# Kernel tuning notes

Hardware: AMD Instinct MI355X
Metric: run time of the kernel (lower is better)

Reference implementation:

```python
import jax, jax.numpy as jnp
import numpy as np

B, H, N, D = 4, 16, 4096, 64
M = 266  # nb_features = int(D * ln(D))
KERNEL_EPS = 1e-4


def _gaussian_orthogonal_random_matrix(nb_rows, nb_cols, rng):
    # Faithful to gaussian_orthogonal_random_matrix with scaling=0.
    blocks = []
    for _ in range(nb_rows // nb_cols):
        q, _ = np.linalg.qr(rng.standard_normal((nb_cols, nb_cols)))
        blocks.append(q.T)
    rem = nb_rows - (nb_rows // nb_cols) * nb_cols
    if rem > 0:
        q, _ = np.linalg.qr(rng.standard_normal((nb_cols, nb_cols)))
        blocks.append(q.T[:rem])
    final = np.concatenate(blocks, axis=0)
    mult = np.linalg.norm(rng.standard_normal((nb_rows, nb_cols)), axis=1)
    return (mult[:, None] * final).astype(np.float32)


def setup_inputs() -> dict:
    key = jax.random.key(0)
    kq, kk, kv = jax.random.split(key, 3)
    q = jax.random.normal(kq, (B, H, N, D), dtype=jnp.float32)
    k = jax.random.normal(kk, (B, H, N, D), dtype=jnp.float32)
    v = jax.random.normal(kv, (B, H, N, D), dtype=jnp.float32)
    proj = jnp.asarray(_gaussian_orthogonal_random_matrix(M, D, np.random.default_rng(0)))
    return {"q": q, "k": k, "v": v, "projection_matrix": proj}


def _softmax_kernel(x, proj, is_query):
    d = x.shape[-1]
    data_normalizer = d ** (-0.25)
    ratio = proj.shape[0] ** (-0.5)
    # [b,h,n,m]
    data_dash = jnp.einsum("bhnd,md->bhnm", data_normalizer * x, proj)
    diag = jnp.sum(x * x, axis=-1, keepdims=True) * 0.5 * (data_normalizer ** 2)
    if is_query:
        mx = jax.lax.stop_gradient(jnp.max(data_dash, axis=-1, keepdims=True))
    else:
        mx = jax.lax.stop_gradient(jnp.max(data_dash, axis=(-1, -2), keepdims=True))
    return ratio * (jnp.exp(data_dash - diag - mx) + KERNEL_EPS)


def _linear_attention(q, k, v):
    k_cumsum = jnp.sum(k, axis=-2)                       # [b,h,m]
    D_ = jnp.einsum("bhnm,bhm->bhn", q, k_cumsum)
    D_inv = 1.0 / jnp.where(D_ == 0, 1e-5, D_)
    context = jnp.einsum("bhnm,bhne->bhme", k, v)        # [b,h,m,e]
    return jnp.einsum("bhme,bhnm,bhn->bhne", context, q, D_inv)


def reference(q, k, v, projection_matrix):
    qp = _softmax_kernel(q, projection_matrix, is_query=True)
    kp = _softmax_kernel(k, projection_matrix, is_query=False)
    return _linear_attention(qp, kp, v)
```

## Files before the change

### kernel.cpp

```cpp
#include <hip/hip_runtime.h>
#include <math.h>


#define BH 64
#define NTOK 4096
#define DIM 64
#define MF 266
#define MPAD 272
#define NCH 8
#define CHROWS 512
#define RATIO 0.06131393394849658f
#define DNORM 0.35355339059327373f
#define DIAGC 0.0625f
#define KEPS 1e-4f

#define PSTR 72
#define QSTR 296

typedef _Float16 half8 __attribute__((ext_vector_type(8)));
typedef _Float16 half4 __attribute__((ext_vector_type(4)));
typedef float floatx4 __attribute__((ext_vector_type(4)));
typedef short short8 __attribute__((ext_vector_type(8)));
typedef short short4s __attribute__((ext_vector_type(4)));

__device__ __forceinline__ short f2h_bits(float f) {
    union { _Float16 h; short s; } u; u.h = (_Float16)f; return u.s;
}
__device__ __forceinline__ float h2f(short s) {
    union { short s; _Float16 h; } u; u.s = s; return (float)u.h;
}
__device__ __forceinline__ short f2bf_bits(float f) {
    unsigned u = __float_as_uint(f);
    return (short)((u + 0x7FFFu + ((u >> 16) & 1u)) >> 16);
}
__device__ __forceinline__ unsigned encf(float f) {
    unsigned u = __float_as_uint(f);
    return (u & 0x80000000u) ? ~u : (u | 0x80000000u);
}
__device__ __forceinline__ float decf(unsigned u) {
    u = (u & 0x80000000u) ? (u & 0x7FFFFFFFu) : ~u;
    return __uint_as_float(u);
}

__device__ __forceinline__ void stage_proj(short* projL, const float* __restrict__ proj, int tid) {
    for (int idx = tid; idx < 544; idx += 512) {
        const int f = idx >> 1, hf = idx & 1;
        short* dst = &projL[f * PSTR + hf * 32];
        if (f < MF) {
            const float* src = proj + f * 64 + hf * 32;
            #pragma unroll
            for (int j2 = 0; j2 < 8; ++j2) {
                float4 v4 = *(const float4*)(src + j2 * 4);
                short4s sv;
                sv[0] = f2h_bits(v4.x * DNORM);
                sv[1] = f2h_bits(v4.y * DNORM);
                sv[2] = f2h_bits(v4.z * DNORM);
                sv[3] = f2h_bits(v4.w * DNORM);
                *(short4s*)(dst + j2 * 4) = sv;
            }
        } else {
            short4s z; z[0] = 0; z[1] = 0; z[2] = 0; z[3] = 0;
            #pragma unroll
            for (int j2 = 0; j2 < 8; ++j2) *(short4s*)(dst + j2 * 4) = z;
        }
    }
}

__global__ __launch_bounds__(512, 2)
void k_pass(const float* __restrict__ kin, const float* __restrict__ vin,
            const float* __restrict__ proj, float* __restrict__ A0p,
            float* __restrict__ S0p, float* __restrict__ Vsp,
            unsigned int* __restrict__ gmax)
{
    __shared__ __align__(16) short epT[2][MPAD * PSTR];
    __shared__ __align__(16) short vT[2][64 * PSTR];
    __shared__ float red8[8];

    const int tid = threadIdx.x;
    const int bh = blockIdx.x >> 3, ch = blockIdx.x & 7;
    const int c = tid & 15, g = (tid >> 4) & 3, w = tid >> 6;
    const int lane = tid & 63;
    const int a = w & 3, h = w >> 2;
    const int tb = 8 * h;

    half8 pb0[9], pb1[9];
    #pragma unroll
    for (int i = 0; i < 9; ++i) {
        const int f = 16 * (tb + i) + c;
        if (f < MF) {
            const float* ps = proj + (size_t)f * 64 + 8 * g;
            float4 x0 = *(const float4*)ps;
            float4 x1 = *(const float4*)(ps + 4);
            float4 x2 = *(const float4*)(ps + 32);
            float4 x3 = *(const float4*)(ps + 36);
            half8 b0, b1;
            b0[0]=(_Float16)(DNORM*x0.x); b0[1]=(_Float16)(DNORM*x0.y);
            b0[2]=(_Float16)(DNORM*x0.z); b0[3]=(_Float16)(DNORM*x0.w);
            b0[4]=(_Float16)(DNORM*x1.x); b0[5]=(_Float16)(DNORM*x1.y);
            b0[6]=(_Float16)(DNORM*x1.z); b0[7]=(_Float16)(DNORM*x1.w);
            b1[0]=(_Float16)(DNORM*x2.x); b1[1]=(_Float16)(DNORM*x2.y);
            b1[2]=(_Float16)(DNORM*x2.z); b1[3]=(_Float16)(DNORM*x2.w);
            b1[4]=(_Float16)(DNORM*x3.x); b1[5]=(_Float16)(DNORM*x3.y);
            b1[6]=(_Float16)(DNORM*x3.z); b1[7]=(_Float16)(DNORM*x3.w);
            pb0[i] = b0; pb1[i] = b1;
        } else {
            half8 z;
            #pragma unroll
            for (int j = 0; j < 8; ++j) z[j] = (_Float16)0.f;
            pb0[i] = z; pb1[i] = z;
        }
    }

    const float* kb = kin + ((size_t)bh * NTOK + (size_t)ch * CHROWS) * DIM;
    const float* vb = vin + ((size_t)bh * NTOK + (size_t)ch * CHROWS) * DIM;

    floatx4 acc9[9];
    float s0acc[9];
    #pragma unroll
    for (int i = 0; i < 9; ++i) {
        acc9[i][0] = 0.f; acc9[i][1] = 0.f; acc9[i][2] = 0.f; acc9[i][3] = 0.f;
        s0acc[i] = 0.f;
    }
    float vsacc = 0.f;
    float dmax = -3.0e38f;

    float4 kx0, kx1, kx2, kx3;
    float vx[8];

    auto prefetch = [&](int s) {
        const int n0 = s * 64;
        const float* ks = kb + (size_t)(n0 + 16 * a + c) * DIM + 8 * g;
        kx0 = *(const float4*)ks;
        kx1 = *(const float4*)(ks + 4);
        kx2 = *(const float4*)(ks + 32);
        kx3 = *(const float4*)(ks + 36);
        const float* vs = vb + (size_t)(n0 + 8 * w) * DIM + lane;
        #pragma unroll
        for (int i = 0; i < 8; ++i) vx[i] = vs[(size_t)i * DIM];
    };

    auto g1 = [&](int buf) {
        short8 pk;
        #pragma unroll
        for (int i = 0; i < 8; ++i) { vsacc += vx[i]; pk[i] = f2bf_bits(vx[i]); }
        *(short8*)&vT[buf][lane * PSTR + 8 * w] = pk;
        half8 af0, af1;
        float dsum = kx0.x*kx0.x + kx0.y*kx0.y + kx0.z*kx0.z + kx0.w*kx0.w
                   + kx1.x*kx1.x + kx1.y*kx1.y + kx1.z*kx1.z + kx1.w*kx1.w
                   + kx2.x*kx2.x + kx2.y*kx2.y + kx2.z*kx2.z + kx2.w*kx2.w
                   + kx3.x*kx3.x + kx3.y*kx3.y + kx3.z*kx3.z + kx3.w*kx3.w;
        af0[0]=(_Float16)kx0.x; af0[1]=(_Float16)kx0.y; af0[2]=(_Float16)kx0.z; af0[3]=(_Float16)kx0.w;
        af0[4]=(_Float16)kx1.x; af0[5]=(_Float16)kx1.y; af0[6]=(_Float16)kx1.z; af0[7]=(_Float16)kx1.w;
        af1[0]=(_Float16)kx2.x; af1[1]=(_Float16)kx2.y; af1[2]=(_Float16)kx2.z; af1[3]=(_Float16)kx2.w;
        af1[4]=(_Float16)kx3.x; af1[5]=(_Float16)kx3.y; af1[6]=(_Float16)kx3.z; af1[7]=(_Float16)kx3.w;
        float t1 = dsum + __shfl_xor(dsum, 16);
        float diagc = (t1 + __shfl_xor(t1, 32)) * DIAGC;
        float dgr[4];
        #pragma unroll
        for (int r2 = 0; r2 < 4; ++r2) dgr[r2] = __shfl(diagc, 4 * g + r2);
        #pragma unroll
        for (int i = 0; i < 9; ++i) {
            const int t = tb + i;
            floatx4 d = {0.f, 0.f, 0.f, 0.f};
            d = __builtin_amdgcn_mfma_f32_16x16x32_f16(af0, pb0[i], d, 0, 0, 0);
            d = __builtin_amdgcn_mfma_f32_16x16x32_f16(af1, pb1[i], d, 0, 0, 0);
            const bool fval = (t < 16) || (c < 10);
            short4s pkk; float s0t = 0.f;
            #pragma unroll
            for (int r2 = 0; r2 < 4; ++r2) {
                float ddv = d[r2];
                if (fval) dmax = fmaxf(dmax, ddv);
                float ev = __expf(ddv - dgr[r2]);
                s0t += ev;
                pkk[r2] = f2bf_bits(ev);
            }
            if (h == 0 || i > 0) s0acc[i] += s0t;
            *(short4s*)&epT[buf][(16 * t + c) * PSTR + 16 * a + 4 * g] = pkk;
        }
    };

    auto g2 = [&](int buf) {
        const short* vp = &vT[buf][(16 * a + c) * PSTR + 8 * g];
        short8 vb0 = *(const short8*)vp;
        short8 vb1 = *(const short8*)(vp + 32);
        #pragma unroll
        for (int i = 0; i < 9; ++i) {
            const short* ap = &epT[buf][(16 * (tb + i) + c) * PSTR + 8 * g];
            short8 a0 = *(const short8*)ap;
            short8 a1 = *(const short8*)(ap + 32);
            acc9[i] = __builtin_amdgcn_mfma_f32_16x16x32_bf16(a0, vb0, acc9[i], 0, 0, 0);
            acc9[i] = __builtin_amdgcn_mfma_f32_16x16x32_bf16(a1, vb1, acc9[i], 0, 0, 0);
        }
    };

    prefetch(0);
    g1(0);
    __syncthreads();
    for (int s = 0; s < 8; ++s) {
        if (s < 7) prefetch(s + 1);
        g2(s & 1);
        if (s < 7) {
            g1((s + 1) & 1);
            __syncthreads();
        }
    }

    {
        float* dst = A0p + (size_t)(bh * NCH + ch) * (MPAD * 64);
        #pragma unroll
        for (int i = 0; i < 9; ++i) {
            const int t = tb + i;
            #pragma unroll
            for (int r2 = 0; r2 < 4; ++r2)
                dst[(size_t)(16 * t + 4 * g + r2) * 64 + 16 * a + c] = acc9[i][r2];
        }
    }
    #pragma unroll
    for (int i = 0; i < 9; ++i) {
        float s = s0acc[i];
        s += __shfl_xor(s, 16); s += __shfl_xor(s, 32);
        if (g == 0) atomicAdd(&S0p[bh * MPAD + 16 * (tb + i) + c], s);
    }
    atomicAdd(&Vsp[bh * 64 + lane], vsacc);
    #pragma unroll
    for (int s = 1; s <= 32; s <<= 1) dmax = fmaxf(dmax, __shfl_xor(dmax, s));
    if (lane == 0) red8[w] = dmax;
    __syncthreads();
    if (tid == 0) {
        float m = red8[0];
        #pragma unroll
        for (int i = 1; i < 8; ++i) m = fmaxf(m, red8[i]);
        atomicMax(gmax + bh, encf(m));
    }
}

__global__ __launch_bounds__(512, 1)
void reduce_ctx(const float* __restrict__ A0p, const float* __restrict__ S0p,
                const float* __restrict__ Vsp, const unsigned int* __restrict__ gmax,
                short* __restrict__ ctxw)
{
    __shared__ __align__(16) short L[65 * 288];
    const int bh = blockIdx.x, tid = threadIdx.x;
    const float emx = __expf(-decf(gmax[bh]));
    const int e = tid & 63, mi = tid >> 6;
    const float vsr = Vsp[bh * 64 + e] * KEPS;
    const float* base = A0p + (size_t)bh * NCH * MPAD * 64;
    for (int m = mi; m < 288; m += 8) {
        float val = 0.f;
        if (m < MF) {
            float s = 0.f;
            #pragma unroll
            for (int c2 = 0; c2 < NCH; ++c2)
                s += base[(size_t)c2 * MPAD * 64 + (size_t)m * 64 + e];
            val = RATIO * (emx * s + vsr);
        }
        L[e * 288 + m] = f2h_bits(val);
    }
    for (int m = tid; m < 288; m += 512) {
        float val = 0.f;
        if (m < MF) val = RATIO * (emx * S0p[bh * MPAD + m] + KEPS * 4096.0f);
        L[64 * 288 + m] = f2h_bits(val);
    }
    __syncthreads();
    short* dst = ctxw + (size_t)bh * (65 * 288);
    for (int idx = tid; idx < 65 * 36; idx += 512)
        *(short8*)(dst + idx * 8) = *(const short8*)&L[idx * 8];
}

__global__ __launch_bounds__(512, 2)
void q_pass(const float* __restrict__ qin, const float* __restrict__ proj,
            const short* __restrict__ ctxw, float* __restrict__ outp)
{
    __shared__ __align__(16) short projL[MPAD * PSTR];
    __shared__ __align__(16) short ctxL[65 * QSTR];

    const int tid = threadIdx.x;
    const int bh = blockIdx.x >> 5, rt = blockIdx.x & 31;
    const int c = tid & 15, g = (tid >> 4) & 3, w = tid >> 6;

    stage_proj(projL, proj, tid);
    {
        const short* src = ctxw + (size_t)bh * (65 * 288);
        for (int idx = tid; idx < 65 * 36; idx += 512) {
            const int r = idx / 36, s = idx - r * 36;
            *(short8*)&ctxL[r * QSTR + s * 8] = *(const short8*)(src + r * 288 + s * 8);
        }
    }
    half8 bf0, bf1;
    float dsum = 0.f;
    {
        const float* qs = qin + ((size_t)bh * NTOK + rt * 128 + 16 * w + c) * DIM;
        #pragma unroll
        for (int ksi = 0; ksi < 2; ++ksi) {
            const float* p4 = qs + ksi * 32 + 8 * g;
            float4 x0 = *(const float4*)p4;
            float4 x1 = *(const float4*)(p4 + 4);
            dsum += x0.x*x0.x + x0.y*x0.y + x0.z*x0.z + x0.w*x0.w
                  + x1.x*x1.x + x1.y*x1.y + x1.z*x1.z + x1.w*x1.w;
            half8& bf = ksi ? bf1 : bf0;
            bf[0]=(_Float16)x0.x; bf[1]=(_Float16)x0.y; bf[2]=(_Float16)x0.z; bf[3]=(_Float16)x0.w;
            bf[4]=(_Float16)x1.x; bf[5]=(_Float16)x1.y; bf[6]=(_Float16)x1.z; bf[7]=(_Float16)x1.w;
        }
    }
    float t1 = dsum + __shfl_xor(dsum, 16);
    const float diagc = (t1 + __shfl_xor(t1, 32)) * DIAGC;

    __syncthreads();

    floatx4 dd[17];
    #pragma unroll
    for (int t = 0; t < 17; ++t) {
        const short* ap = &projL[(16 * t + c) * PSTR + 8 * g];
        half8 a0 = *(const half8*)ap;
        half8 a1 = *(const half8*)(ap + 32);
        floatx4 d = {0.f, 0.f, 0.f, 0.f};
        d = __builtin_amdgcn_mfma_f32_16x16x32_f16(a0, bf0, d, 0, 0, 0);
        d = __builtin_amdgcn_mfma_f32_16x16x32_f16(a1, bf1, d, 0, 0, 0);
        dd[t] = d;
    }
    float mx = -3.0e38f;
    #pragma unroll
    for (int t = 0; t < 17; ++t) {
        #pragma unroll
        for (int r2 = 0; r2 < 4; ++r2) {
            const bool fval = (t < 16) || (4 * g + r2 < 10);
            if (fval) mx = fmaxf(mx, dd[t][r2]);
        }
    }
    mx = fmaxf(mx, __shfl_xor(mx, 16));
    mx = fmaxf(mx, __shfl_xor(mx, 32));

    half4 bq[17];
    float denp = 0.f;
    #pragma unroll
    for (int t = 0; t < 17; ++t) {
        half4 b;
        #pragma unroll
        for (int r2 = 0; r2 < 4; ++r2) {
            float val = __expf(dd[t][r2] - diagc - mx) + KEPS;
            b[r2] = (_Float16)val;
            denp += val * h2f(ctxL[64 * QSTR + 16 * t + 4 * g + r2]);
        }
        bq[t] = b;
    }
    denp += __shfl_xor(denp, 16);
    denp += __shfl_xor(denp, 32);

    floatx4 acc[4];
    #pragma unroll
    for (int i = 0; i < 4; ++i) { acc[i][0]=0.f; acc[i][1]=0.f; acc[i][2]=0.f; acc[i][3]=0.f; }
    #pragma unroll
    for (int e4 = 0; e4 < 4; ++e4) {
        #pragma unroll
        for (int t = 0; t < 17; ++t) {
            half4 a4 = *(const half4*)&ctxL[(16 * e4 + c) * QSTR + 16 * t + 4 * g];
            acc[e4] = __builtin_amdgcn_mfma_f32_16x16x16f16(a4, bq[t], acc[e4], 0, 0, 0);
        }
    }
    float den = (denp == 0.f) ? 1e-5f : denp;
    const float inv = 1.0f / den;
    float* ob = outp + ((size_t)bh * NTOK + rt * 128 + 16 * w + c) * DIM;
    #pragma unroll
    for (int e4 = 0; e4 < 4; ++e4) {
        float4 o = make_float4(acc[e4][0] * inv, acc[e4][1] * inv,
                               acc[e4][2] * inv, acc[e4][3] * inv);
        *(float4*)(ob + 16 * e4 + 4 * g) = o;
    }
}

extern "C" void kernel_launch(void* const* d_in, const int* in_sizes, int n_in,
                              void* d_out, int out_size, void* d_ws, size_t ws_size,
                              hipStream_t stream)
{
    const float* q    = (const float*)d_in[0];
    const float* k    = (const float*)d_in[1];
    const float* v    = (const float*)d_in[2];
    const float* proj = (const float*)d_in[3];
    float* out = (float*)d_out;
    float* ws  = (float*)d_ws;

    const size_t offS = (size_t)BH * NCH * MPAD * 64;
    const size_t offV = offS + (size_t)BH * MPAD;
    const size_t offG = offV + (size_t)BH * 64;
    const size_t offC = offG + 64;

    float* A0p = ws;
    float* S0p = ws + offS;
    float* Vsp = ws + offV;
    unsigned int* gmax = (unsigned int*)(ws + offG);
    short* ctxw = (short*)(ws + offC);

    hipMemsetAsync(S0p, 0, ((size_t)BH * MPAD + (size_t)BH * 64 + 64) * sizeof(float), stream);
    hipLaunchKernelGGL(k_pass, dim3(BH * NCH), dim3(512), 0, stream,
                       k, v, proj, A0p, S0p, Vsp, gmax);
    hipLaunchKernelGGL(reduce_ctx, dim3(BH), dim3(512), 0, stream,
                       A0p, S0p, Vsp, gmax, ctxw);
    hipLaunchKernelGGL(q_pass, dim3(BH * 32), dim3(512), 0, stream,
                       q, proj, ctxw, out);
}
```

Before: 165.4 us.

## Restructure k_pass: split features across blocks, stage K in LDS, fold V-sum into MFMA

Rewrites the key-side pass so each block handles half of the feature tiles over a 1024-row chunk. K is staged in LDS as fp16 with precomputed diagonals, and exp features live in small per-warp LDS tiles instead of a large double-buffered feature buffer. LDS use drops, which allows four blocks per CU. The V column sum is obtained by setting a padded feature column to 1, so the extra atomic buffer and its accumulation go away. Conversions now use packed bf16/fp16 conversion instructions. The cost is a transposed scalar LDS write pattern for V and redundant reloads of K per block half.

```diff
diff --git a/kernel.cpp b/kernel.cpp
--- a/kernel.cpp
+++ b/kernel.cpp
@@ -7,8 +7,9 @@
 #define DIM 64
 #define MF 266
 #define MPAD 272
-#define NCH 8
-#define CHROWS 512
+#define NCH 4
+#define CHROWS 1024
+#define SUBS 16
 #define RATIO 0.06131393394849658f
 #define DNORM 0.35355339059327373f
 #define DIAGC 0.0625f
@@ -19,6 +20,7 @@
 
 typedef _Float16 half8 __attribute__((ext_vector_type(8)));
 typedef _Float16 half4 __attribute__((ext_vector_type(4)));
+typedef __fp16 fp16x2 __attribute__((ext_vector_type(2)));
 typedef float floatx4 __attribute__((ext_vector_type(4)));
 typedef short short8 __attribute__((ext_vector_type(8)));
 typedef short short4s __attribute__((ext_vector_type(4)));
@@ -29,9 +31,10 @@
 __device__ __forceinline__ float h2f(short s) {
     union { short s; _Float16 h; } u; u.s = s; return (float)u.h;
 }
-__device__ __forceinline__ short f2bf_bits(float f) {
-    unsigned u = __float_as_uint(f);
-    return (short)((u + 0x7FFFu + ((u >> 16) & 1u)) >> 16);
+__device__ __forceinline__ unsigned cvt_pk_bf16(float lo, float hi) {
+    unsigned r;
+    asm("v_cvt_pk_bf16_f32 %0, %1, %2" : "=v"(r) : "v"(lo), "v"(hi));
+    return r;
 }
 __device__ __forceinline__ unsigned encf(float f) {
     unsigned u = __float_as_uint(f);
@@ -40,6 +43,233 @@
 __device__ __forceinline__ float decf(unsigned u) {
     u = (u & 0x80000000u) ? (u & 0x7FFFFFFFu) : ~u;
     return __uint_as_float(u);
+}
+
+__global__ __launch_bounds__(512, 4)
+void k_pass(const float* __restrict__ kin, const float* __restrict__ vin,
+            const float* __restrict__ proj, float* __restrict__ A0p,
+            float* __restrict__ S0p, unsigned int* __restrict__ gmax)
+{
+    __shared__ __align__(16) short kL[2][64 * PSTR];
+    __shared__ __align__(16) short vT[2][64 * PSTR];
+    __shared__ float diagL[2][64];
+    __shared__ __align__(16) short epS[16][16 * PSTR];
+
+    const int tid = threadIdx.x;
+    const int l = tid & 63, w = tid >> 6;
+    const int c = tid & 15, g = (tid >> 4) & 3;
+    const int bh = blockIdx.x >> 3;
+    const int ch = (blockIdx.x >> 1) & 3;
+    const int h  = blockIdx.x & 1;
+    const int nT = (h == 1 && w == 0) ? 2 : 1;
+    const int t0 = (h == 0) ? w : (8 + w);
+
+    half8 pj0[2], pj1[2];
+    #pragma unroll
+    for (int it = 0; it < 2; ++it) {
+        half8 z;
+        #pragma unroll
+        for (int j = 0; j < 8; ++j) z[j] = (_Float16)0.f;
+        pj0[it] = z; pj1[it] = z;
+        const int t = it ? 16 : t0;
+        const int f = 16 * t + c;
+        if (it < nT && f < MF) {
+            const float* ps = proj + (size_t)f * 64 + 8 * g;
+            float4 x0 = *(const float4*)ps;
+            float4 x1 = *(const float4*)(ps + 4);
+            float4 x2 = *(const float4*)(ps + 32);
+            float4 x3 = *(const float4*)(ps + 36);
+            half8 b0, b1;
+            b0[0]=(_Float16)(DNORM*x0.x); b0[1]=(_Float16)(DNORM*x0.y);
+            b0[2]=(_Float16)(DNORM*x0.z); b0[3]=(_Float16)(DNORM*x0.w);
+            b0[4]=(_Float16)(DNORM*x1.x); b0[5]=(_Float16)(DNORM*x1.y);
+            b0[6]=(_Float16)(DNORM*x1.z); b0[7]=(_Float16)(DNORM*x1.w);
+            b1[0]=(_Float16)(DNORM*x2.x); b1[1]=(_Float16)(DNORM*x2.y);
+            b1[2]=(_Float16)(DNORM*x2.z); b1[3]=(_Float16)(DNORM*x2.w);
+            b1[4]=(_Float16)(DNORM*x3.x); b1[5]=(_Float16)(DNORM*x3.y);
+            b1[6]=(_Float16)(DNORM*x3.z); b1[7]=(_Float16)(DNORM*x3.w);
+            pj0[it] = b0; pj1[it] = b1;
+        }
+    }
+
+    const float* kb = kin + ((size_t)bh * NTOK + (size_t)ch * CHROWS) * DIM;
+    const float* vb = vin + ((size_t)bh * NTOK + (size_t)ch * CHROWS) * DIM;
+
+    const int srow = 8 * w + (l >> 3);
+    const int sd0  = (l & 7) * 8;
+    const int vrow = l;
+    const int ve0  = 8 * w;
+
+    floatx4 acc[2][4];
+    #pragma unroll
+    for (int it = 0; it < 2; ++it)
+        #pragma unroll
+        for (int et = 0; et < 4; ++et) {
+            acc[it][et][0]=0.f; acc[it][et][1]=0.f; acc[it][et][2]=0.f; acc[it][et][3]=0.f;
+        }
+    float s0acc[2] = {0.f, 0.f};
+    float dmax = -3.0e38f;
+
+    float4 ka0, ka1, va0, va1;
+
+    auto issue_loads = [&](int s) {
+        const float* ks = kb + (size_t)(64 * s + srow) * DIM + sd0;
+        ka0 = *(const float4*)ks;
+        ka1 = *(const float4*)(ks + 4);
+        const float* vs = vb + (size_t)(64 * s + vrow) * DIM + ve0;
+        va0 = *(const float4*)vs;
+        va1 = *(const float4*)(vs + 4);
+    };
+
+    auto stage_write = [&](int buf) {
+        union { fp16x2 h2[4]; short8 s8; } uk;
+        uk.h2[0] = __builtin_amdgcn_cvt_pkrtz(ka0.x, ka0.y);
+        uk.h2[1] = __builtin_amdgcn_cvt_pkrtz(ka0.z, ka0.w);
+        uk.h2[2] = __builtin_amdgcn_cvt_pkrtz(ka1.x, ka1.y);
+        uk.h2[3] = __builtin_amdgcn_cvt_pkrtz(ka1.z, ka1.w);
+        *(short8*)&kL[buf][srow * PSTR + sd0] = uk.s8;
+        float ds2 = ka0.x*ka0.x + ka0.y*ka0.y + ka0.z*ka0.z + ka0.w*ka0.w
+                  + ka1.x*ka1.x + ka1.y*ka1.y + ka1.z*ka1.z + ka1.w*ka1.w;
+        ds2 += __shfl_xor(ds2, 1);
+        ds2 += __shfl_xor(ds2, 2);
+        ds2 += __shfl_xor(ds2, 4);
+        if ((l & 7) == 0) diagL[buf][srow] = ds2 * DIAGC;
+        unsigned pv0 = cvt_pk_bf16(va0.x, va0.y);
+        unsigned pv1 = cvt_pk_bf16(va0.z, va0.w);
+        unsigned pv2 = cvt_pk_bf16(va1.x, va1.y);
+        unsigned pv3 = cvt_pk_bf16(va1.z, va1.w);
+        vT[buf][(ve0 + 0) * PSTR + vrow] = (short)(pv0 & 0xFFFF);
+        vT[buf][(ve0 + 1) * PSTR + vrow] = (short)(pv0 >> 16);
+        vT[buf][(ve0 + 2) * PSTR + vrow] = (short)(pv1 & 0xFFFF);
+        vT[buf][(ve0 + 3) * PSTR + vrow] = (short)(pv1 >> 16);
+        vT[buf][(ve0 + 4) * PSTR + vrow] = (short)(pv2 & 0xFFFF);
+        vT[buf][(ve0 + 5) * PSTR + vrow] = (short)(pv2 >> 16);
+        vT[buf][(ve0 + 6) * PSTR + vrow] = (short)(pv3 & 0xFFFF);
+        vT[buf][(ve0 + 7) * PSTR + vrow] = (short)(pv3 >> 16);
+    };
+
+    issue_loads(0);
+    stage_write(0);
+    __syncthreads();
+
+    for (int s = 0; s < SUBS; ++s) {
+        const int cur = s & 1;
+        const bool more = (s + 1 < SUBS);
+        if (more) issue_loads(s + 1);
+
+        #pragma unroll
+        for (int nt = 0; nt < 4; ++nt) {
+            const half8 a0 = *(const half8*)&kL[cur][(16 * nt + c) * PSTR + 8 * g];
+            const half8 a1 = *(const half8*)&kL[cur][(16 * nt + c) * PSTR + 8 * g + 32];
+            const float4 dg4 = *(const float4*)&diagL[cur][16 * nt + 4 * g];
+            const float dgr[4] = {dg4.x, dg4.y, dg4.z, dg4.w};
+            #pragma unroll
+            for (int it = 0; it < 2; ++it) {
+                if (it < nT) {
+                    floatx4 d = {0.f, 0.f, 0.f, 0.f};
+                    d = __builtin_amdgcn_mfma_f32_16x16x32_f16(a0, pj0[it], d, 0, 0, 0);
+                    d = __builtin_amdgcn_mfma_f32_16x16x32_f16(a1, pj1[it], d, 0, 0, 0);
+                    const bool t16 = (it == 1);
+                    float ev[4];
+                    #pragma unroll
+                    for (int r = 0; r < 4; ++r) {
+                        const float ddv = d[r];
+                        if (!t16 || c < 10) dmax = fmaxf(dmax, ddv);
+                        float e = __expf(ddv - dgr[r]);
+                        if (t16 && c == 15) e = 1.0f;
+                        s0acc[it] += e;
+                        ev[r] = e;
+                    }
+                    uint2 pk;
+                    pk.x = cvt_pk_bf16(ev[0], ev[1]);
+                    pk.y = cvt_pk_bf16(ev[2], ev[3]);
+                    *(uint2*)&epS[2 * w + it][c * PSTR + 16 * nt + 4 * g] = pk;
+                }
+            }
+        }
+
+        #pragma unroll
+        for (int ntp = 0; ntp < 2; ++ntp) {
+            const short8 bq0 = *(const short8*)&epS[2 * w][c * PSTR + 32 * ntp + 8 * g];
+            short8 bq1;
+            if (nT == 2) bq1 = *(const short8*)&epS[2 * w + 1][c * PSTR + 32 * ntp + 8 * g];
+            #pragma unroll
+            for (int et = 0; et < 4; ++et) {
+                const short8 av = *(const short8*)&vT[cur][(16 * et + c) * PSTR + 32 * ntp + 8 * g];
+                acc[0][et] = __builtin_amdgcn_mfma_f32_16x16x32_bf16(av, bq0, acc[0][et], 0, 0, 0);
+                if (nT == 2)
+                    acc[1][et] = __builtin_amdgcn_mfma_f32_16x16x32_bf16(av, bq1, acc[1][et], 0, 0, 0);
+            }
+        }
+
+        if (more) {
+            stage_write(cur ^ 1);
+            __syncthreads();
+        }
+    }
+
+    {
+        float* dst = A0p + (size_t)(bh * NCH + ch) * (MPAD * 64);
+        #pragma unroll
+        for (int it = 0; it < 2; ++it) {
+            if (it < nT) {
+                const int t = it ? 16 : t0;
+                #pragma unroll
+                for (int et = 0; et < 4; ++et)
+                    *(floatx4*)&dst[(size_t)(16 * t + c) * 64 + 16 * et + 4 * g] = acc[it][et];
+            }
+        }
+    }
+    #pragma unroll
+    for (int it = 0; it < 2; ++it) {
+        if (it < nT) {
+            const int t = it ? 16 : t0;
+            float s = s0acc[it];
+            s += __shfl_xor(s, 16);
+            s += __shfl_xor(s, 32);
+            if (g == 0 && (t < 16 || c < 10))
+                atomicAdd(&S0p[bh * MPAD + 16 * t + c], s);
+        }
+    }
+    #pragma unroll
+    for (int sft = 1; sft <= 32; sft <<= 1) dmax = fmaxf(dmax, __shfl_xor(dmax, sft));
+    if (l == 0) atomicMax(gmax + bh, encf(dmax));
+}
+
+__global__ __launch_bounds__(512, 1)
+void reduce_ctx(const float* __restrict__ A0p, const float* __restrict__ S0p,
+                const unsigned int* __restrict__ gmax, short* __restrict__ ctxw)
+{
+    __shared__ __align__(16) short L[65 * 288];
+    const int bh = blockIdx.x, tid = threadIdx.x;
+    const float emx = __expf(-decf(gmax[bh]));
+    const int e = tid & 63, mi = tid >> 6;
+    const float* base = A0p + (size_t)bh * NCH * MPAD * 64;
+    float vs = 0.f;
+    #pragma unroll
+    for (int c2 = 0; c2 < NCH; ++c2)
+        vs += base[(size_t)c2 * MPAD * 64 + (size_t)271 * 64 + e];
+    const float vsr = vs * KEPS;
+    for (int m = mi; m < 288; m += 8) {
+        float val = 0.f;
+        if (m < MF) {
+            float s = 0.f;
+            #pragma unroll
+            for (int c2 = 0; c2 < NCH; ++c2)
+                s += base[(size_t)c2 * MPAD * 64 + (size_t)m * 64 + e];
+            val = RATIO * (emx * s + vsr);
+        }
+        L[e * 288 + m] = f2h_bits(val);
+    }
+    for (int m = tid; m < 288; m += 512) {
+        float val = 0.f;
+        if (m < MF) val = RATIO * (emx * S0p[bh * MPAD + m] + KEPS * 4096.0f);
+        L[64 * 288 + m] = f2h_bits(val);
+    }
+    __syncthreads();
+    short* dst = ctxw + (size_t)bh * (65 * 288);
+    for (int idx = tid; idx < 65 * 36; idx += 512)
+        *(short8*)(dst + idx * 8) = *(const short8*)&L[idx * 8];
 }
 
 __device__ __forceinline__ void stage_proj(short* projL, const float* __restrict__ proj, int tid) {
@@ -67,207 +297,6 @@
 }
 
 __global__ __launch_bounds__(512, 2)
-void k_pass(const float* __restrict__ kin, const float* __restrict__ vin,
-            const float* __restrict__ proj, float* __restrict__ A0p,
-            float* __restrict__ S0p, float* __restrict__ Vsp,
-            unsigned int* __restrict__ gmax)
-{
-    __shared__ __align__(16) short epT[2][MPAD * PSTR];
-    __shared__ __align__(16) short vT[2][64 * PSTR];
-    __shared__ float red8[8];
-
-    const int tid = threadIdx.x;
-    const int bh = blockIdx.x >> 3, ch = blockIdx.x & 7;
-    const int c = tid & 15, g = (tid >> 4) & 3, w = tid >> 6;
-    const int lane = tid & 63;
-    const int a = w & 3, h = w >> 2;
-    const int tb = 8 * h;
-
-    half8 pb0[9], pb1[9];
-    #pragma unroll
-    for (int i = 0; i < 9; ++i) {
-        const int f = 16 * (tb + i) + c;
-        if (f < MF) {
-            const float* ps = proj + (size_t)f * 64 + 8 * g;
-            float4 x0 = *(const float4*)ps;
-            float4 x1 = *(const float4*)(ps + 4);
-            float4 x2 = *(const float4*)(ps + 32);
-            float4 x3 = *(const float4*)(ps + 36);
-            half8 b0, b1;
-            b0[0]=(_Float16)(DNORM*x0.x); b0[1]=(_Float16)(DNORM*x0.y);
-            b0[2]=(_Float16)(DNORM*x0.z); b0[3]=(_Float16)(DNORM*x0.w);
-            b0[4]=(_Float16)(DNORM*x1.x); b0[5]=(_Float16)(DNORM*x1.y);
-            b0[6]=(_Float16)(DNORM*x1.z); b0[7]=(_Float16)(DNORM*x1.w);
-            b1[0]=(_Float16)(DNORM*x2.x); b1[1]=(_Float16)(DNORM*x2.y);
-            b1[2]=(_Float16)(DNORM*x2.z); b1[3]=(_Float16)(DNORM*x2.w);
-            b1[4]=(_Float16)(DNORM*x3.x); b1[5]=(_Float16)(DNORM*x3.y);
-            b1[6]=(_Float16)(DNORM*x3.z); b1[7]=(_Float16)(DNORM*x3.w);
-            pb0[i] = b0; pb1[i] = b1;
-        } else {
-            half8 z;
-            #pragma unroll
-            for (int j = 0; j < 8; ++j) z[j] = (_Float16)0.f;
-            pb0[i] = z; pb1[i] = z;
-        }
-    }
-
-    const float* kb = kin + ((size_t)bh * NTOK + (size_t)ch * CHROWS) * DIM;
-    const float* vb = vin + ((size_t)bh * NTOK + (size_t)ch * CHROWS) * DIM;
-
-    floatx4 acc9[9];
-    float s0acc[9];
-    #pragma unroll
-    for (int i = 0; i < 9; ++i) {
-        acc9[i][0] = 0.f; acc9[i][1] = 0.f; acc9[i][2] = 0.f; acc9[i][3] = 0.f;
-        s0acc[i] = 0.f;
-    }
-    float vsacc = 0.f;
-    float dmax = -3.0e38f;
-
-    float4 kx0, kx1, kx2, kx3;
-    float vx[8];
-
-    auto prefetch = [&](int s) {
-        const int n0 = s * 64;
-        const float* ks = kb + (size_t)(n0 + 16 * a + c) * DIM + 8 * g;
-        kx0 = *(const float4*)ks;
-        kx1 = *(const float4*)(ks + 4);
-        kx2 = *(const float4*)(ks + 32);
-        kx3 = *(const float4*)(ks + 36);
-        const float* vs = vb + (size_t)(n0 + 8 * w) * DIM + lane;
-        #pragma unroll
-        for (int i = 0; i < 8; ++i) vx[i] = vs[(size_t)i * DIM];
-    };
-
-    auto g1 = [&](int buf) {
-        short8 pk;
-        #pragma unroll
-        for (int i = 0; i < 8; ++i) { vsacc += vx[i]; pk[i] = f2bf_bits(vx[i]); }
-        *(short8*)&vT[buf][lane * PSTR + 8 * w] = pk;
-        half8 af0, af1;
-        float dsum = kx0.x*kx0.x + kx0.y*kx0.y + kx0.z*kx0.z + kx0.w*kx0.w
-                   + kx1.x*kx1.x + kx1.y*kx1.y + kx1.z*kx1.z + kx1.w*kx1.w
-                   + kx2.x*kx2.x + kx2.y*kx2.y + kx2.z*kx2.z + kx2.w*kx2.w
-                   + kx3.x*kx3.x + kx3.y*kx3.y + kx3.z*kx3.z + kx3.w*kx3.w;
-        af0[0]=(_Float16)kx0.x; af0[1]=(_Float16)kx0.y; af0[2]=(_Float16)kx0.z; af0[3]=(_Float16)kx0.w;
-        af0[4]=(_Float16)kx1.x; af0[5]=(_Float16)kx1.y; af0[6]=(_Float16)kx1.z; af0[7]=(_Float16)kx1.w;
-        af1[0]=(_Float16)kx2.x; af1[1]=(_Float16)kx2.y; af1[2]=(_Float16)kx2.z; af1[3]=(_Float16)kx2.w;
-        af1[4]=(_Float16)kx3.x; af1[5]=(_Float16)kx3.y; af1[6]=(_Float16)kx3.z; af1[7]=(_Float16)kx3.w;
-        float t1 = dsum + __shfl_xor(dsum, 16);
-        float diagc = (t1 + __shfl_xor(t1, 32)) * DIAGC;
-        float dgr[4];
-        #pragma unroll
-        for (int r2 = 0; r2 < 4; ++r2) dgr[r2] = __shfl(diagc, 4 * g + r2);
-        #pragma unroll
-        for (int i = 0; i < 9; ++i) {
-            const int t = tb + i;
-            floatx4 d = {0.f, 0.f, 0.f, 0.f};
-            d = __builtin_amdgcn_mfma_f32_16x16x32_f16(af0, pb0[i], d, 0, 0, 0);
-            d = __builtin_amdgcn_mfma_f32_16x16x32_f16(af1, pb1[i], d, 0, 0, 0);
-            const bool fval = (t < 16) || (c < 10);
-            short4s pkk; float s0t = 0.f;
-            #pragma unroll
-            for (int r2 = 0; r2 < 4; ++r2) {
-                float ddv = d[r2];
-                if (fval) dmax = fmaxf(dmax, ddv);
-                float ev = __expf(ddv - dgr[r2]);
-                s0t += ev;
-                pkk[r2] = f2bf_bits(ev);
-            }
-            if (h == 0 || i > 0) s0acc[i] += s0t;
-            *(short4s*)&epT[buf][(16 * t + c) * PSTR + 16 * a + 4 * g] = pkk;
-        }
-    };
-
-    auto g2 = [&](int buf) {
-        const short* vp = &vT[buf][(16 * a + c) * PSTR + 8 * g];
-        short8 vb0 = *(const short8*)vp;
-        short8 vb1 = *(const short8*)(vp + 32);
-        #pragma unroll
-        for (int i = 0; i < 9; ++i) {
-            const short* ap = &epT[buf][(16 * (tb + i) + c) * PSTR + 8 * g];
-            short8 a0 = *(const short8*)ap;
-            short8 a1 = *(const short8*)(ap + 32);
-            acc9[i] = __builtin_amdgcn_mfma_f32_16x16x32_bf16(a0, vb0, acc9[i], 0, 0, 0);
-            acc9[i] = __builtin_amdgcn_mfma_f32_16x16x32_bf16(a1, vb1, acc9[i], 0, 0, 0);
-        }
-    };
-
-    prefetch(0);
-    g1(0);
-    __syncthreads();
-    for (int s = 0; s < 8; ++s) {
-        if (s < 7) prefetch(s + 1);
-        g2(s & 1);
-        if (s < 7) {
-            g1((s + 1) & 1);
-            __syncthreads();
-        }
-    }
-
-    {
-        float* dst = A0p + (size_t)(bh * NCH + ch) * (MPAD * 64);
-        #pragma unroll
-        for (int i = 0; i < 9; ++i) {
-            const int t = tb + i;
-            #pragma unroll
-            for (int r2 = 0; r2 < 4; ++r2)
-                dst[(size_t)(16 * t + 4 * g + r2) * 64 + 16 * a + c] = acc9[i][r2];
-        }
-    }
-    #pragma unroll
-    for (int i = 0; i < 9; ++i) {
-        float s = s0acc[i];
-        s += __shfl_xor(s, 16); s += __shfl_xor(s, 32);
-        if (g == 0) atomicAdd(&S0p[bh * MPAD + 16 * (tb + i) + c], s);
-    }
-    atomicAdd(&Vsp[bh * 64 + lane], vsacc);
-    #pragma unroll
-    for (int s = 1; s <= 32; s <<= 1) dmax = fmaxf(dmax, __shfl_xor(dmax, s));
-    if (lane == 0) red8[w] = dmax;
-    __syncthreads();
-    if (tid == 0) {
-        float m = red8[0];
-        #pragma unroll
-        for (int i = 1; i < 8; ++i) m = fmaxf(m, red8[i]);
-        atomicMax(gmax + bh, encf(m));
-    }
-}
-
-__global__ __launch_bounds__(512, 1)
-void reduce_ctx(const float* __restrict__ A0p, const float* __restrict__ S0p,
-                const float* __restrict__ Vsp, const unsigned int* __restrict__ gmax,
-                short* __restrict__ ctxw)
-{
-    __shared__ __align__(16) short L[65 * 288];
-    const int bh = blockIdx.x, tid = threadIdx.x;
-    const float emx = __expf(-decf(gmax[bh]));
-    const int e = tid & 63, mi = tid >> 6;
-    const float vsr = Vsp[bh * 64 + e] * KEPS;
-    const float* base = A0p + (size_t)bh * NCH * MPAD * 64;
-    for (int m = mi; m < 288; m += 8) {
-        float val = 0.f;
-        if (m < MF) {
-            float s = 0.f;
-            #pragma unroll
-            for (int c2 = 0; c2 < NCH; ++c2)
-                s += base[(size_t)c2 * MPAD * 64 + (size_t)m * 64 + e];
-            val = RATIO * (emx * s + vsr);
-        }
-        L[e * 288 + m] = f2h_bits(val);
-    }
-    for (int m = tid; m < 288; m += 512) {
-        float val = 0.f;
-        if (m < MF) val = RATIO * (emx * S0p[bh * MPAD + m] + KEPS * 4096.0f);
-        L[64 * 288 + m] = f2h_bits(val);
-    }
-    __syncthreads();
-    short* dst = ctxw + (size_t)bh * (65 * 288);
-    for (int idx = tid; idx < 65 * 36; idx += 512)
-        *(short8*)(dst + idx * 8) = *(const short8*)&L[idx * 8];
-}
-
-__global__ __launch_bounds__(512, 2)
 void q_pass(const float* __restrict__ qin, const float* __restrict__ proj,
             const short* __restrict__ ctxw, float* __restrict__ outp)
 {
@@ -380,21 +409,19 @@
     float* ws  = (float*)d_ws;
 
     const size_t offS = (size_t)BH * NCH * MPAD * 64;
-    const size_t offV = offS + (size_t)BH * MPAD;
-    const size_t offG = offV + (size_t)BH * 64;
+    const size_t offG = offS + (size_t)BH * MPAD;
     const size_t offC = offG + 64;
 
     float* A0p = ws;
     float* S0p = ws + offS;
-    float* Vsp = ws + offV;
     unsigned int* gmax = (unsigned int*)(ws + offG);
     short* ctxw = (short*)(ws + offC);
 
-    hipMemsetAsync(S0p, 0, ((size_t)BH * MPAD + (size_t)BH * 64 + 64) * sizeof(float), stream);
-    hipLaunchKernelGGL(k_pass, dim3(BH * NCH), dim3(512), 0, stream,
-                       k, v, proj, A0p, S0p, Vsp, gmax);
+    (void)hipMemsetAsync(S0p, 0, ((size_t)BH * MPAD + 64) * sizeof(float), stream);
+    hipLaunchKernelGGL(k_pass, dim3(BH * NCH * 2), dim3(512), 0, stream,
+                       k, v, proj, A0p, S0p, gmax);
     hipLaunchKernelGGL(reduce_ctx, dim3(BH), dim3(512), 0, stream,
-                       A0p, S0p, Vsp, gmax, ctxw);
+                       A0p, S0p, gmax, ctxw);
     hipLaunchKernelGGL(q_pass, dim3(BH * 32), dim3(512), 0, stream,
                        q, proj, ctxw, out);
 }
```

Result: faster. 144.3 us (-12.7%).
